# Optimization experiments

Hardware: AMD Instinct MI355X
Metric: run time of the kernel (lower is better)

Reference implementation:

```python
import jax, jax.numpy as jnp
import numpy as np

B = 4096      # batch
GH, GW = 13, 3
G = GH * GW   # 39 social grid cells
K = 20        # occupied cells per sample
T = 16        # history length
N = B * K     # total neighbors
FUT = 24      # decode horizon


def _lin_init(key, out_d, in_d):
    s = 1.0 / np.sqrt(in_d)
    kw, kb = jax.random.split(key)
    w = jax.random.uniform(kw, (out_d, in_d), jnp.float32, -s, s)
    b = jax.random.uniform(kb, (out_d,), jnp.float32, -s, s)
    return w, b


def setup_inputs() -> dict:
    key = jax.random.key(0)
    ks = jax.random.split(key, 12)
    x = jax.random.normal(ks[0], (B, 12, 24, 2), jnp.float32)
    beta = jax.random.uniform(ks[1], (B,), jnp.float32)
    context = jax.random.normal(ks[2], (T, B, 2), jnp.float32)
    nbrs = jax.random.normal(ks[3], (T, N, 2), jnp.float32)
    # first K of G grid cells occupied for every sample (deterministic pattern)
    cell = jnp.arange(G) < K                                  # (G,)
    mask = jnp.broadcast_to(cell[None, :, None], (B, G, 64)).reshape(B, GH, GW, 64)
    ip_w, ip_b = _lin_init(ks[4], 32, 2)
    enc_wih, enc_bih = _lin_init(ks[5], 4 * 64, 32)
    enc_whh, enc_bhh = _lin_init(ks[6], 4 * 64, 64)
    dyn_w, dyn_b = _lin_init(ks[7], 32, 64)
    lin1_w, lin1_b = _lin_init(ks[8], 1, 96)
    dec_wih, dec_bih = _lin_init(ks[9], 4 * 256, 96)
    dec_whh, dec_bhh = _lin_init(ks[10], 4 * 256, 256)
    op_w, op_b = _lin_init(ks[11], 5, 256)
    return dict(x=x, beta=beta, context=context, nbrs=nbrs, mask=mask,
                ip_w=ip_w, ip_b=ip_b, enc_wih=enc_wih, enc_whh=enc_whh,
                enc_bih=enc_bih, enc_bhh=enc_bhh, dyn_w=dyn_w, dyn_b=dyn_b,
                lin1_w=lin1_w, lin1_b=lin1_b, dec_wih=dec_wih, dec_whh=dec_whh,
                dec_bih=dec_bih, dec_bhh=dec_bhh, op_w=op_w, op_b=op_b)


def _lstm(seq, wih, whh, bih, bhh, hid):
    # seq: (T, n, in). torch gate order i, f, g, o. Returns (all_h, last_h).
    n = seq.shape[1]
    h0 = jnp.zeros((n, hid), seq.dtype)
    b = bih + bhh
    def step(carry, xt):
        h, c = carry
        g = xt @ wih.T + h @ whh.T + b
        i, f, gg, o = jnp.split(g, 4, axis=-1)
        c = jax.nn.sigmoid(f) * c + jax.nn.sigmoid(i) * jnp.tanh(gg)
        h = jax.nn.sigmoid(o) * jnp.tanh(c)
        return (h, c), h
    (h, c), hs = jax.lax.scan(step, (h0, h0), seq)
    return hs, h


def _lrelu(v):
    return jnp.where(v >= 0, v, 0.1 * v)


def _forward(x, beta, context, nbrs, mask,
             ip_w, ip_b, enc_wih, enc_whh, enc_bih, enc_bhh,
             dyn_w, dyn_b, lin1_w, lin1_b,
             dec_wih, dec_whh, dec_bih, dec_bhh, op_w, op_b):
    # --- encode ego history ---
    ctx_in = _lrelu(context @ ip_w.T + ip_b)            # (T, B, 32)
    _, hist_h = _lstm(ctx_in, enc_wih, enc_whh, enc_bih, enc_bhh, 64)  # (B, 64)
    hist_enc_one = _lrelu(hist_h @ dyn_w.T + dyn_b)     # (B, 32)
    # --- encode neighbors ---
    nbr_in = _lrelu(nbrs @ ip_w.T + ip_b)               # (T, N, 32)
    _, nbrs_h = _lstm(nbr_in, enc_wih, enc_whh, enc_bih, enc_bhh, 64)  # (N, 64)
    # --- masked_scatter_: place nbrs_h rows into True grid cells (row-major) ---
    b_, g_ = mask.shape[0], mask.shape[1] * mask.shape[2]
    cell_mask = mask.reshape(b_ * g_, mask.shape[3])[:, 0]            # (B*G,) bool
    idx = jnp.clip(jnp.cumsum(cell_mask.astype(jnp.int32)) - 1, 0, nbrs_h.shape[0] - 1)
    soc = jnp.where(cell_mask[:, None], nbrs_h[idx], 0.0).reshape(b_, g_, 64)
    mask_enc = cell_mask.reshape(b_, g_)                # (B, G)
    # --- tanh attention over grid cells ---
    hist_t = jnp.broadcast_to(hist_enc_one[:, None, :], (b_, g_, 32))
    new_hs = jnp.tanh(jnp.concatenate([hist_t, soc], axis=2))         # (B, G, 96)
    e = (new_hs @ lin1_w.T + lin1_b)[..., 0]            # (B, G)
    e = jnp.where(mask_enc, e, -1e9)
    attn = jax.nn.softmax(e, axis=1)
    enc = jnp.einsum('bg,bgc->bc', attn, soc)           # (B, 64)
    ctx = jnp.concatenate([hist_enc_one, enc], axis=1)  # (B, 96)
    # --- decode: repeat over 24 steps through dec_lstm ---
    dec_in = jnp.broadcast_to(ctx[None], (FUT, b_, 96))
    h_dec, _ = _lstm(dec_in, dec_wih, dec_whh, dec_bih, dec_bhh, 256)  # (24, B, 256)
    fut = h_dec @ op_w.T + op_b                         # (24, B, 5)
    mu = fut[..., :2]
    sig = jnp.exp(fut[..., 2:4])
    rho = jnp.tanh(fut[..., 4:5])
    out = jnp.concatenate([mu, sig, rho], axis=-1)      # (24, B, 5)
    return jnp.transpose(out, (1, 0, 2))                # (B, 24, 5)


def reference(x, beta, context, nbrs, mask,
              ip_w, ip_b, enc_wih, enc_whh, enc_bih, enc_bhh,
              dyn_w, dyn_b, lin1_w, lin1_b,
              dec_wih, dec_whh, dec_bih, dec_bhh, op_w, op_b):
    return _forward(x, beta, context, nbrs, mask,
                    ip_w, ip_b, enc_wih, enc_whh, enc_bih, enc_bhh,
                    dyn_w, dyn_b, lin1_w, lin1_b,
                    dec_wih, dec_whh, dec_bih, dec_bhh, op_w, op_b)
```

## Files before the change

kernel.cpp:

```cpp
#include <hip/hip_runtime.h>


#define S_TOT 86016
#define NB    4096
#define NNB   81920
#define TT    16
#define NFUT  24
#define HXS   104
#define L2E   1.44269504088896f

typedef __attribute__((ext_vector_type(8)))  short short8v;
typedef __attribute__((ext_vector_type(16))) float f32x16;

__device__ __forceinline__ float rcpf(float x) { return __builtin_amdgcn_rcpf(x); }
__device__ __forceinline__ float sigm2(float a)  { return rcpf(1.0f + exp2f(-a)); }
__device__ __forceinline__ float tanh2(float a)  { return 1.0f - 2.0f * rcpf(exp2f(a) + 1.0f); }
__device__ __forceinline__ float tanhx(float x)  { return tanh2(x * (2.0f * L2E)); }
__device__ __forceinline__ float lrelu(float v)  { return v >= 0.0f ? v : 0.1f * v; }
__device__ __forceinline__ short f2bf(float f) {
    unsigned u = __float_as_uint(f);
    unsigned r = (u + 0x7fffu + ((u >> 16) & 1u)) >> 16;
    return (short)r;
}

__global__ __launch_bounds__(64) void k_pack_encB(
    const float* __restrict__ wih, const float* __restrict__ whh,
    const float* __restrict__ bih, const float* __restrict__ bhh,
    short* __restrict__ pB, float* __restrict__ pbias)
{
    const int fi = blockIdx.x;
    const int cc = fi % 6, gg = fi / 6;
    const int gate = gg & 3, H = gg >> 2;
    const int lane = threadIdx.x;
    const int row  = gate * 64 + H * 32 + (lane & 31);
    const float sc = (gate == 2) ? 2.0f * L2E : L2E;
    short8v v;
#pragma unroll
    for (int u = 0; u < 8; u++) {
        const int k = cc * 16 + (lane >> 5) * 8 + u;
        const float f = (k < 32) ? wih[row * 32 + k] : whh[row * 64 + (k - 32)];
        v[u] = f2bf(f * sc);
    }
    *(short8v*)&pB[((size_t)fi * 64 + lane) * 8] = v;
    if (cc == 0 && lane < 32)
        pbias[H * 128 + gate * 32 + lane] = (bih[row] + bhh[row]) * sc;
}

__global__ __launch_bounds__(128) void k_encoder(
    const float* __restrict__ ctx_raw,
    const float* __restrict__ nbr_raw,
    const float* __restrict__ ipw, const float* __restrict__ ipb,
    const short* __restrict__ pB, const float* __restrict__ pbias,
    float* __restrict__ hfin)
{
    __shared__ short hx2[2 * 32 * HXS];
    const int tid  = threadIdx.x;
    const int lane = tid & 63;
    const int H    = __builtin_amdgcn_readfirstlane(tid >> 6);
    const int seq_base = blockIdx.x * 32;
    const bool is_hist = (seq_base < NB);

    short8v Bf[4][6];
#pragma unroll
    for (int gate = 0; gate < 4; gate++)
#pragma unroll
        for (int cc = 0; cc < 6; cc++)
            Bf[gate][cc] = *(const short8v*)
                &pB[(((size_t)(H * 4 + gate) * 6 + cc) * 64 + lane) * 8];

    float b4[4];
#pragma unroll
    for (int gate = 0; gate < 4; gate++)
        b4[gate] = pbias[H * 128 + gate * 32 + (lane & 31)];

    {
        short8v z;
#pragma unroll
        for (int u = 0; u < 8; u++) z[u] = 0;
        for (int i = tid; i < 32 * 8; i += 128)
            *(short8v*)&hx2[(i >> 3) * HXS + 32 + (i & 7) * 8] = z;
    }

    const int sx = seq_base + (tid & 31);
    float2 f2;
    {
        const float* rp = is_hist ? &ctx_raw[(size_t)sx * 2]
                                  : &nbr_raw[(size_t)(sx - NB) * 2];
        f2 = *(const float2*)rp;
        const int k0 = (tid >> 5) * 8;
        short8v xv;
#pragma unroll
        for (int u = 0; u < 8; u++) {
            const int xj = k0 + u;
            xv[u] = f2bf(lrelu(ipb[xj] + ipw[xj * 2] * f2.x + ipw[xj * 2 + 1] * f2.y));
        }
        *(short8v*)&hx2[(tid & 31) * HXS + k0] = xv;
    }
    __syncthreads();

    float cst[16];
#pragma unroll
    for (int r = 0; r < 16; r++) cst[r] = 0.0f;

    const int aoff = (lane & 31) * HXS + (lane >> 5) * 8;
    const int hcol = 32 + H * 32 + (lane & 31);

#pragma unroll 1
    for (int t = 0; t < TT; t++) {
        short* cur = hx2 + (t & 1) * (32 * HXS);
        short* nxt = hx2 + ((t + 1) & 1) * (32 * HXS);

        float2 f2n = f2;
        if (t < TT - 1) {
            const float* rp = is_hist
                ? &ctx_raw[((size_t)(t + 1) * NB + sx) * 2]
                : &nbr_raw[((size_t)(t + 1) * NNB + (sx - NB)) * 2];
            f2n = *(const float2*)rp;
        }

        short8v Af[6];
#pragma unroll
        for (int cc = 0; cc < 6; cc++)
            Af[cc] = *(const short8v*)&cur[aoff + cc * 16];

        f32x16 C[4];
#pragma unroll
        for (int gate = 0; gate < 4; gate++)
#pragma unroll
            for (int r = 0; r < 16; r++) C[gate][r] = b4[gate];

#pragma unroll
        for (int cc = 0; cc < 6; cc++)
#pragma unroll
            for (int gate = 0; gate < 4; gate++)
                C[gate] = __builtin_amdgcn_mfma_f32_32x32x16_bf16(
                    Af[cc], Bf[gate][cc], C[gate], 0, 0, 0);

        float hn[16];
#pragma unroll
        for (int r = 0; r < 16; r++) {
            const float iv = sigm2(C[0][r]);
            const float fv = sigm2(C[1][r]);
            const float gv = tanh2(C[2][r]);
            const float ov = sigm2(C[3][r]);
            const float cn = fv * cst[r] + iv * gv;
            cst[r] = cn;
            hn[r] = ov * tanhx(cn);
        }

        if (t < TT - 1) {
#pragma unroll
            for (int r = 0; r < 16; r++) {
                const int row = (r & 3) + 8 * (r >> 2) + 4 * (lane >> 5);
                nxt[row * HXS + hcol] = f2bf(hn[r]);
            }
            const int k0 = (tid >> 5) * 8;
            short8v xv;
#pragma unroll
            for (int u = 0; u < 8; u++) {
                const int xj = k0 + u;
                xv[u] = f2bf(lrelu(ipb[xj] + ipw[xj * 2] * f2n.x + ipw[xj * 2 + 1] * f2n.y));
            }
            *(short8v*)&nxt[(tid & 31) * HXS + k0] = xv;
            __syncthreads();
            f2 = f2n;
        } else {
#pragma unroll
            for (int r = 0; r < 16; r++) {
                const int row = (r & 3) + 8 * (r >> 2) + 4 * (lane >> 5);
                hfin[(size_t)(seq_base + row) * 64 + H * 32 + (lane & 31)] = hn[r];
            }
        }
    }
}

__global__ __launch_bounds__(256) void k_attn(
    const float* __restrict__ h_enc,
    const float* __restrict__ dynw, const float* __restrict__ dynb,
    const float* __restrict__ l1w,  const float* __restrict__ l1b,
    float* __restrict__ ctx)
{
    const int b   = blockIdx.x;
    const int tid = threadIdx.x;
    __shared__ float sh_he[32];
    __shared__ float sh_soc[20][65];
    __shared__ float sh_e[20];

    if (tid < 32) {
        float a = dynb[tid];
        const float* w  = &dynw[tid * 64];
        const float* hb = &h_enc[(size_t)b * 64];
#pragma unroll 8
        for (int k = 0; k < 64; k++) a += w[k] * hb[k];
        a = lrelu(a);
        sh_he[tid] = a;
        ctx[b * 96 + tid] = a;
    }
    for (int idx = tid; idx < 20 * 64; idx += 256) {
        const int g = idx >> 6, k = idx & 63;
        sh_soc[g][k] = h_enc[(size_t)(NB + b * 20 + g) * 64 + k];
    }
    __syncthreads();

    if (tid < 20) {
        float e = l1b[0];
#pragma unroll
        for (int m = 0; m < 32; m++) e += l1w[m] * tanhx(sh_he[m]);
#pragma unroll 8
        for (int k = 0; k < 64; k++) e += l1w[32 + k] * tanhx(sh_soc[tid][k]);
        sh_e[tid] = e;
    }
    __syncthreads();

    if (tid < 64) {
        float mx = -1e30f;
#pragma unroll
        for (int g = 0; g < 20; g++) mx = fmaxf(mx, sh_e[g]);
        float wgt[20];
        float sm = 0.0f;
#pragma unroll
        for (int g = 0; g < 20; g++) { wgt[g] = exp2f((sh_e[g] - mx) * L2E); sm += wgt[g]; }
        const float inv = 1.0f / sm;
        float a = 0.0f;
#pragma unroll
        for (int g = 0; g < 20; g++) a += wgt[g] * sh_soc[g][tid];
        ctx[b * 96 + 32 + tid] = a * inv;
    }
}

__global__ __launch_bounds__(256) void k_pack_decB(
    const float* __restrict__ whh,
    const float* __restrict__ opw,
    short* __restrict__ pBd, short* __restrict__ opwB)
{
    const int bid  = blockIdx.x;
    const int tid  = threadIdx.x;
    const int lane = tid & 63;
    if (bid < 128) {
        const int gate = tid >> 6;
        const int hg = bid >> 4, cc = bid & 15;
        const int row  = gate * 256 + hg * 32 + (lane & 31);
        const int kb   = cc * 16 + (lane >> 5) * 8;
        const float sc = (gate == 2) ? 2.0f * L2E : L2E;
        short8v v;
#pragma unroll
        for (int u = 0; u < 8; u++) v[u] = f2bf(whh[row * 256 + kb + u] * sc);
        *(short8v*)&pBd[((size_t)(bid * 4 + gate) * 64 + lane) * 8] = v;
    } else if (tid < 64) {
        const int cc = bid - 128;
        const int n  = lane & 31, kb = cc * 16 + (lane >> 5) * 8;
        short8v v;
#pragma unroll
        for (int u = 0; u < 8; u++)
            v[u] = (n < 5) ? f2bf(opw[n * 256 + kb + u]) : (short)0;
        *(short8v*)&opwB[(cc * 64 + lane) * 8] = v;
    }
}

__global__ __launch_bounds__(256) void k_gx(
    const float* __restrict__ ctx,
    const float* __restrict__ wih,
    const float* __restrict__ bih, const float* __restrict__ bhh,
    float* __restrict__ pgx)
{
    const int lane = threadIdx.x & 63;
    const int s    = blockIdx.x * 64 + lane;
    const int jq   = __builtin_amdgcn_readfirstlane(blockIdx.y * 4 + (threadIdx.x >> 6));
    const int j0   = jq * 4;
    float acc[4];
#pragma unroll
    for (int d = 0; d < 4; d++) acc[d] = bih[j0 + d] + bhh[j0 + d];
    const float* c = &ctx[(size_t)s * 96];
    for (int k0 = 0; k0 < 96; k0 += 8) {
        float cb[8];
#pragma unroll
        for (int u = 0; u < 8; u++) cb[u] = c[k0 + u];
#pragma unroll
        for (int d = 0; d < 4; d++) {
            const float* w = &wih[(j0 + d) * 96 + k0];
#pragma unroll
            for (int u = 0; u < 8; u++) acc[d] += w[u] * cb[u];
        }
    }
#pragma unroll
    for (int d = 0; d < 4; d++) {
        const int row = j0 + d;
        const int g = row >> 8, j = row & 255;
        const float sc = (g == 2) ? 2.0f * L2E : L2E;
        pgx[(((size_t)s << 8) + j) * 4 + g] = acc[d] * sc;
    }
}

__global__ __launch_bounds__(512, 2) void k_dec_persist(
    const float* __restrict__ pgx,
    const short* __restrict__ pBd,
    const short* __restrict__ opwB,
    const float* __restrict__ opb,
    float* __restrict__ out)
{
    __shared__ short hbuf[2][32 * 256];
    const int tid  = threadIdx.x;
    const int lane = tid & 63;
    const int w    = __builtin_amdgcn_readfirstlane(tid >> 6);
    const int Ab   = blockIdx.x * 32;
    const int n    = lane & 31;
    const int hl   = lane >> 5;
    const bool headw = (w == 0);

    const short* wb = pBd + (size_t)w * 32768 + (size_t)lane * 8;
    const short* ob = opwB + (size_t)lane * 8;

    float cst[16];
#pragma unroll
    for (int r = 0; r < 16; r++) cst[r] = 0.0f;

#pragma unroll 1
    for (int t = 0; t < NFUT; t++) {
        const char* cur = (const char*)hbuf[t & 1];
        char* nxt       = (char*)hbuf[(t + 1) & 1];

        f32x16 C[4], Ch;
#pragma unroll
        for (int g = 0; g < 4; g++)
#pragma unroll
            for (int r = 0; r < 16; r++) C[g][r] = 0.0f;
#pragma unroll
        for (int r = 0; r < 16; r++) Ch[r] = 0.0f;

        if (t > 0) {
#pragma unroll 4
            for (int cc = 0; cc < 16; cc++) {
                const int abyte = n * 512 + ((cc * 32 + hl * 16) ^ ((n & 7) << 4));
                const short8v Af = *(const short8v*)(cur + abyte);
#pragma unroll
                for (int g = 0; g < 4; g++) {
                    const short8v Bf = *(const short8v*)&wb[(size_t)(cc * 4 + g) * 512];
                    C[g] = __builtin_amdgcn_mfma_f32_32x32x16_bf16(Af, Bf, C[g], 0, 0, 0);
                }
                if (headw) {
                    const short8v Of = *(const short8v*)&ob[(size_t)cc * 512];
                    Ch = __builtin_amdgcn_mfma_f32_32x32x16_bf16(Af, Of, Ch, 0, 0, 0);
                }
            }
        }

#pragma unroll
        for (int r = 0; r < 16; r++) {
            const int al = (r & 3) + 8 * (r >> 2) + 4 * hl;
            const float4 g4 = *(const float4*)
                &pgx[(((size_t)(Ab + al) << 8) + w * 32 + n) * 4];
            const float iv = sigm2(C[0][r] + g4.x);
            const float fv = sigm2(C[1][r] + g4.y);
            const float gv = tanh2(C[2][r] + g4.z);
            const float ov = sigm2(C[3][r] + g4.w);
            const float cn = fv * cst[r] + iv * gv;
            cst[r] = cn;
            const int hbyte = al * 512 + (((w * 32 + n) * 2) ^ ((al & 7) << 4));
            *(short*)(nxt + hbyte) = f2bf(ov * tanhx(cn));
        }

        if (t > 0 && headw && n < 5) {
            const float obias = opb[n];
#pragma unroll
            for (int r = 0; r < 16; r++) {
                const int agent = Ab + (r & 3) + 8 * (r >> 2) + 4 * hl;
                float v = Ch[r] + obias;
                if (n == 2 || n == 3) v = exp2f(v * L2E);
                else if (n == 4) v = tanhx(v);
                out[(size_t)agent * (NFUT * 5) + (t - 1) * 5 + n] = v;
            }
        }

        __syncthreads();
    }

    if (headw) {
        const char* cur = (const char*)hbuf[NFUT & 1];
        f32x16 Ch;
#pragma unroll
        for (int r = 0; r < 16; r++) Ch[r] = 0.0f;
#pragma unroll 4
        for (int cc = 0; cc < 16; cc++) {
            const int abyte = n * 512 + ((cc * 32 + hl * 16) ^ ((n & 7) << 4));
            const short8v Af = *(const short8v*)(cur + abyte);
            const short8v Of = *(const short8v*)&ob[(size_t)cc * 512];
            Ch = __builtin_amdgcn_mfma_f32_32x32x16_bf16(Af, Of, Ch, 0, 0, 0);
        }
        if (n < 5) {
            const float obias = opb[n];
#pragma unroll
            for (int r = 0; r < 16; r++) {
                const int agent = Ab + (r & 3) + 8 * (r >> 2) + 4 * hl;
                float v = Ch[r] + obias;
                if (n == 2 || n == 3) v = exp2f(v * L2E);
                else if (n == 4) v = tanhx(v);
                out[(size_t)agent * (NFUT * 5) + (NFUT - 1) * 5 + n] = v;
            }
        }
    }
}

extern "C" void kernel_launch(void* const* d_in, const int* in_sizes, int n_in,
                              void* d_out, int out_size, void* d_ws, size_t ws_size,
                              hipStream_t stream)
{
    const float* ctx_raw = (const float*)d_in[2];
    const float* nbr_raw = (const float*)d_in[3];
    const float* ipw     = (const float*)d_in[5];
    const float* ipb     = (const float*)d_in[6];
    const float* enc_wih = (const float*)d_in[7];
    const float* enc_whh = (const float*)d_in[8];
    const float* enc_bih = (const float*)d_in[9];
    const float* enc_bhh = (const float*)d_in[10];
    const float* dynw    = (const float*)d_in[11];
    const float* dynb    = (const float*)d_in[12];
    const float* l1w     = (const float*)d_in[13];
    const float* l1b     = (const float*)d_in[14];
    const float* dec_wih = (const float*)d_in[15];
    const float* dec_whh = (const float*)d_in[16];
    const float* dec_bih = (const float*)d_in[17];
    const float* dec_bhh = (const float*)d_in[18];
    const float* opw     = (const float*)d_in[19];
    const float* opb     = (const float*)d_in[20];
    float* out = (float*)d_out;

    char* pc = (char*)d_ws;
    float* hfin  = (float*)pc; pc += (size_t)S_TOT * 64 * 4;
    float* ctxb  = (float*)pc; pc += (size_t)NB * 96 * 4;
    float* pgx   = (float*)pc; pc += (size_t)NB * 1024 * 4;
    float* pbias = (float*)pc; pc += 256 * 4;
    short* pB    = (short*)pc; pc += (size_t)48 * 64 * 8 * 2;
    short* pBd   = (short*)pc; pc += (size_t)8 * 16 * 4 * 64 * 8 * 2;
    short* opwB  = (short*)pc; pc += (size_t)16 * 64 * 8 * 2;

    k_pack_encB<<<dim3(48), 64, 0, stream>>>(enc_wih, enc_whh, enc_bih, enc_bhh,
                                             pB, pbias);
    k_pack_decB<<<dim3(144), 256, 0, stream>>>(dec_whh, opw, pBd, opwB);

    k_encoder<<<dim3(S_TOT / 32), 128, 0, stream>>>(
        ctx_raw, nbr_raw, ipw, ipb, pB, pbias, hfin);

    k_attn<<<dim3(NB), 256, 0, stream>>>(hfin, dynw, dynb, l1w, l1b, ctxb);

    k_gx<<<dim3(NB / 64, 64), 256, 0, stream>>>(ctxb, dec_wih, dec_bih, dec_bhh, pgx);

    k_dec_persist<<<dim3(NB / 32), 512, 0, stream>>>(pgx, pBd, opwB, opb, out);
}
```

Baseline: 581.9 us.

## Widen encoder blocks to 64 sequences and software-pipeline decoder MFMA operand loads

```diff
diff --git a/kernel.cpp b/kernel.cpp
--- a/kernel.cpp
+++ b/kernel.cpp
@@ -46,18 +46,20 @@
         pbias[H * 128 + gate * 32 + lane] = (bih[row] + bhh[row]) * sc;
 }
 
-__global__ __launch_bounds__(128) void k_encoder(
+__global__ __launch_bounds__(256, 2) void k_encoder(
     const float* __restrict__ ctx_raw,
     const float* __restrict__ nbr_raw,
     const float* __restrict__ ipw, const float* __restrict__ ipb,
     const short* __restrict__ pB, const float* __restrict__ pbias,
     float* __restrict__ hfin)
 {
-    __shared__ short hx2[2 * 32 * HXS];
+    __shared__ short hx2[2 * 64 * HXS];
     const int tid  = threadIdx.x;
     const int lane = tid & 63;
-    const int H    = __builtin_amdgcn_readfirstlane(tid >> 6);
-    const int seq_base = blockIdx.x * 32;
+    const int w    = __builtin_amdgcn_readfirstlane(tid >> 6);
+    const int H    = w >> 1;
+    const int M0   = (w & 1) * 32;
+    const int seq_base = blockIdx.x * 64;
     const bool is_hist = (seq_base < NB);
 
     short8v Bf[4][6];
@@ -77,24 +79,24 @@
         short8v z;
 #pragma unroll
         for (int u = 0; u < 8; u++) z[u] = 0;
-        for (int i = tid; i < 32 * 8; i += 128)
+        for (int i = tid; i < 64 * 8; i += 256)
             *(short8v*)&hx2[(i >> 3) * HXS + 32 + (i & 7) * 8] = z;
     }
 
-    const int sx = seq_base + (tid & 31);
+    const int sx = seq_base + (tid & 63);
     float2 f2;
     {
         const float* rp = is_hist ? &ctx_raw[(size_t)sx * 2]
                                   : &nbr_raw[(size_t)(sx - NB) * 2];
         f2 = *(const float2*)rp;
-        const int k0 = (tid >> 5) * 8;
+        const int k0 = (tid >> 6) * 8;
         short8v xv;
 #pragma unroll
         for (int u = 0; u < 8; u++) {
             const int xj = k0 + u;
             xv[u] = f2bf(lrelu(ipb[xj] + ipw[xj * 2] * f2.x + ipw[xj * 2 + 1] * f2.y));
         }
-        *(short8v*)&hx2[(tid & 31) * HXS + k0] = xv;
+        *(short8v*)&hx2[(tid & 63) * HXS + k0] = xv;
     }
     __syncthreads();
 
@@ -102,13 +104,13 @@
 #pragma unroll
     for (int r = 0; r < 16; r++) cst[r] = 0.0f;
 
-    const int aoff = (lane & 31) * HXS + (lane >> 5) * 8;
+    const int aoff = (M0 + (lane & 31)) * HXS + (lane >> 5) * 8;
     const int hcol = 32 + H * 32 + (lane & 31);
 
 #pragma unroll 1
     for (int t = 0; t < TT; t++) {
-        short* cur = hx2 + (t & 1) * (32 * HXS);
-        short* nxt = hx2 + ((t + 1) & 1) * (32 * HXS);
+        short* cur = hx2 + (t & 1) * (64 * HXS);
+        short* nxt = hx2 + ((t + 1) & 1) * (64 * HXS);
 
         float2 f2n = f2;
         if (t < TT - 1) {
@@ -152,23 +154,23 @@
 #pragma unroll
             for (int r = 0; r < 16; r++) {
                 const int row = (r & 3) + 8 * (r >> 2) + 4 * (lane >> 5);
-                nxt[row * HXS + hcol] = f2bf(hn[r]);
-            }
-            const int k0 = (tid >> 5) * 8;
+                nxt[(M0 + row) * HXS + hcol] = f2bf(hn[r]);
+            }
+            const int k0 = (tid >> 6) * 8;
             short8v xv;
 #pragma unroll
             for (int u = 0; u < 8; u++) {
                 const int xj = k0 + u;
                 xv[u] = f2bf(lrelu(ipb[xj] + ipw[xj * 2] * f2n.x + ipw[xj * 2 + 1] * f2n.y));
             }
-            *(short8v*)&nxt[(tid & 31) * HXS + k0] = xv;
+            *(short8v*)&nxt[(tid & 63) * HXS + k0] = xv;
             __syncthreads();
             f2 = f2n;
         } else {
 #pragma unroll
             for (int r = 0; r < 16; r++) {
                 const int row = (r & 3) + 8 * (r >> 2) + 4 * (lane >> 5);
-                hfin[(size_t)(seq_base + row) * 64 + H * 32 + (lane & 31)] = hn[r];
+                hfin[(size_t)(seq_base + M0 + row) * 64 + H * 32 + (lane & 31)] = hn[r];
             }
         }
     }
@@ -328,19 +330,51 @@
         for (int r = 0; r < 16; r++) Ch[r] = 0.0f;
 
         if (t > 0) {
-#pragma unroll 4
+            short8v Wf[4][4];
+#pragma unroll
+            for (int p = 0; p < 4; p++)
+#pragma unroll
+                for (int g = 0; g < 4; g++)
+                    Wf[p][g] = *(const short8v*)&wb[(size_t)(p * 4 + g) * 512];
+
+            short8v Ofb[2];
+            if (headw) {
+                Ofb[0] = *(const short8v*)&ob[0];
+                Ofb[1] = *(const short8v*)&ob[512];
+            }
+
+            short8v Afb[2];
+            Afb[0] = *(const short8v*)(cur + n * 512 + ((hl * 16) ^ ((n & 7) << 4)));
+            Afb[1] = *(const short8v*)(cur + n * 512 + ((32 + hl * 16) ^ ((n & 7) << 4)));
+
+#pragma unroll
             for (int cc = 0; cc < 16; cc++) {
-                const int abyte = n * 512 + ((cc * 32 + hl * 16) ^ ((n & 7) << 4));
-                const short8v Af = *(const short8v*)(cur + abyte);
-#pragma unroll
-                for (int g = 0; g < 4; g++) {
-                    const short8v Bf = *(const short8v*)&wb[(size_t)(cc * 4 + g) * 512];
-                    C[g] = __builtin_amdgcn_mfma_f32_32x32x16_bf16(Af, Bf, C[g], 0, 0, 0);
+                const int slot = cc & 3;
+                const short8v Af = Afb[cc & 1];
+                const short8v W0 = Wf[slot][0], W1 = Wf[slot][1],
+                              W2 = Wf[slot][2], W3 = Wf[slot][3];
+                short8v Of;
+                if (headw) Of = Ofb[cc & 1];
+
+                if (cc < 12) {
+#pragma unroll
+                    for (int g = 0; g < 4; g++)
+                        Wf[slot][g] = *(const short8v*)
+                            &wb[(size_t)((cc + 4) * 4 + g) * 512];
                 }
-                if (headw) {
-                    const short8v Of = *(const short8v*)&ob[(size_t)cc * 512];
+                if (cc < 14) {
+                    Afb[cc & 1] = *(const short8v*)
+                        (cur + n * 512 + (((cc + 2) * 32 + hl * 16) ^ ((n & 7) << 4)));
+                    if (headw)
+                        Ofb[cc & 1] = *(const short8v*)&ob[(size_t)(cc + 2) * 512];
+                }
+
+                C[0] = __builtin_amdgcn_mfma_f32_32x32x16_bf16(Af, W0, C[0], 0, 0, 0);
+                C[1] = __builtin_amdgcn_mfma_f32_32x32x16_bf16(Af, W1, C[1], 0, 0, 0);
+                C[2] = __builtin_amdgcn_mfma_f32_32x32x16_bf16(Af, W2, C[2], 0, 0, 0);
+                C[3] = __builtin_amdgcn_mfma_f32_32x32x16_bf16(Af, W3, C[3], 0, 0, 0);
+                if (headw)
                     Ch = __builtin_amdgcn_mfma_f32_32x32x16_bf16(Af, Of, Ch, 0, 0, 0);
-                }
             }
         }
 
@@ -437,7 +471,7 @@
                                              pB, pbias);
     k_pack_decB<<<dim3(144), 256, 0, stream>>>(dec_whh, opw, pBd, opwB);
 
-    k_encoder<<<dim3(S_TOT / 32), 128, 0, stream>>>(
+    k_encoder<<<dim3(S_TOT / 64), 256, 0, stream>>>(
         ctx_raw, nbr_raw, ipw, ipb, pB, pbias, hfin);
 
     k_attn<<<dim3(NB), 256, 0, stream>>>(hfin, dynw, dynb, l1w, l1b, ctxb);
```

Result: slower. 1.205 ms (+107.2%).
